# Performance work log

Measured on AMD Instinct MI355X. Metric: run time of the kernel, lower is better.

## Reference

```python
import jax, jax.numpy as jnp
import numpy as np

# ---- config (from init_kwargs) ----
PRE_NMS_THRESH = 0.05
K = 200                    # pre_nms_top_n (fixed-size top-k for jit)
NUM_CLASSES = 80
FPN_STRIDE = 8
MASK_SCALE_FACTOR = 2
MASK_STRIDE = FPN_STRIDE / MASK_SCALE_FACTOR  # 4.0
IMG_H, IMG_W = 768, 768


def setup_inputs() -> dict:
    key = jax.random.key(0)
    ks = jax.random.split(key, 6)
    N, C, H, W, DIM = 2, NUM_CLASSES, 96, 96, 32
    # FCOS-style locations for the stride-8 level: center of each cell
    ys, xs = jnp.meshgrid(jnp.arange(H, dtype=jnp.float32),
                          jnp.arange(W, dtype=jnp.float32), indexing='ij')
    locations = jnp.stack([xs.reshape(-1), ys.reshape(-1)], axis=1) * FPN_STRIDE + FPN_STRIDE // 2
    return {
        'locations': locations,                                                 # [HW, 2]
        'box_cls': jax.random.normal(ks[0], (N, C, H, W), jnp.float32) - 2.0,   # mostly below thresh
        'box_regression': jax.random.uniform(ks[1], (N, 4, H, W), jnp.float32) * 100.0,
        'centerness': jax.random.normal(ks[2], (N, 1, H, W), jnp.float32),
        'proposal_embed': jax.random.normal(ks[3], (N, DIM, H, W), jnp.float32),
        'proposal_margin': jax.random.uniform(ks[4], (N, 1, H, W), jnp.float32, minval=0.1, maxval=2.0),
        'pixel_embed': jax.random.normal(ks[5], (N, DIM, 192, 192), jnp.float32),
    }


def reference(locations, box_cls, box_regression, centerness,
              proposal_embed, proposal_margin, pixel_embed):
    N, C, H, W = box_cls.shape
    DIM = proposal_embed.shape[1]
    o_h = pixel_embed.shape[2] * MASK_SCALE_FACTOR
    o_w = pixel_embed.shape[3] * MASK_SCALE_FACTOR

    # interpolate(pixel_embed, size=(o_h, o_w), mode='bilinear', align_corners=False)
    pix_up = jax.image.resize(pixel_embed, (N, DIM, o_h, o_w), method='bilinear')

    # NCHW -> [N, HW, C] flattening (matches permute(0,2,3,1).reshape)
    scores = jax.nn.sigmoid(jnp.transpose(box_cls.reshape(N, C, H * W), (0, 2, 1)))   # [N, HW, C]
    ctr = jax.nn.sigmoid(centerness.reshape(N, H * W))                                # [N, HW]
    reg = jnp.transpose(box_regression.reshape(N, 4, H * W), (0, 2, 1))               # [N, HW, 4]
    emb = jnp.transpose(proposal_embed.reshape(N, DIM, H * W), (0, 2, 1))             # [N, HW, DIM]
    mar = proposal_margin.reshape(N, H * W)                                           # [N, HW]

    xs = jnp.arange(o_w, dtype=jnp.float32)
    ys = jnp.arange(o_h, dtype=jnp.float32)

    def per_image(s, c, r, e, m, pix):
        # threshold + centerness-weighted score; invalid candidates rank last
        cand = s > PRE_NMS_THRESH                       # [HW, C]
        sc = s * c[:, None]                             # [HW, C]
        flat = jnp.where(cand, sc, -1.0).reshape(-1)    # [HW*C]
        topv, topi = jax.lax.top_k(flat, K)             # fixed-size top-k
        loc_idx = topi // C                             # [K]
        labels = topi % C + 1                           # [K]
        valid = topv > 0.0                              # padded slots when < K candidates

        # box decode: [x - l, y - t, x + r, y + b], clipped to image
        loc = locations[loc_idx]                        # [K, 2]
        rr = r[loc_idx]                                 # [K, 4]
        x1 = jnp.clip(loc[:, 0] - rr[:, 0], 0.0, IMG_W - 1)
        y1 = jnp.clip(loc[:, 1] - rr[:, 1], 0.0, IMG_H - 1)
        x2 = jnp.clip(loc[:, 0] + rr[:, 2], 0.0, IMG_W - 1)
        y2 = jnp.clip(loc[:, 1] + rr[:, 3], 0.0, IMG_H - 1)
        boxes = jnp.stack([x1, y1, x2, y2], axis=1)     # [K, 4]

        # boxes_to_masks at mask stride: binary inside-box masks [K, o_h, o_w]
        mb = boxes / MASK_STRIDE
        in_x = (xs[None, :] >= mb[:, 0:1]) & (xs[None, :] <= mb[:, 2:3])  # [K, o_w]
        in_y = (ys[None, :] >= mb[:, 1:2]) & (ys[None, :] <= mb[:, 3:4])  # [K, o_h]
        box_mask = in_y[:, :, None] & in_x[:, None, :]

        # pixel-embed distance mask: exp(-||pix - e_k||^2 * margin_k)
        ek = e[loc_idx]                                 # [K, DIM]
        mk = m[loc_idx]                                 # [K]
        p = pix.reshape(DIM, o_h * o_w)                 # [DIM, P]
        d2 = (jnp.sum(ek * ek, axis=1)[:, None]
              + jnp.sum(p * p, axis=0)[None, :]
              - 2.0 * ek @ p)                           # [K, P] via GEMM
        prob = jnp.exp(-d2 * mk[:, None]).reshape(K, o_h, o_w)
        masks = prob * box_mask.astype(prob.dtype) * valid[:, None, None].astype(prob.dtype)
        return masks

    masks = jax.vmap(per_image)(scores, ctr, reg, emb, mar, pix_up)  # [N, K, o_h, o_w]
    return masks
```

## Files before the change

### kernel.cpp

```cpp
#include <hip/hip_runtime.h>
#include <cmath>


namespace {
constexpr int NIMG = 2;
constexpr int NC   = 80;
constexpr int NHW  = 96 * 96;
constexpr int NCHW = NC * NHW;
constexpr int NDIM = 32;
constexpr int PH = 192, PW = 192;
constexpr int OH = 384, OW = 384;
constexpr int KTOP = 200;
constexpr int CAP = 4096;
constexpr int MCAP = 1024;
constexpr int LCAP = 512;
constexpr float PRE_THRESH = 0.05f;
constexpr unsigned KEY_ZERO = 0x80000000u;
constexpr float IMG_MAX = 767.0f;

constexpr int NBOX = NIMG * KTOP;
constexpr int ZTILES = 3;
constexpr int NZB = NBOX * ZTILES;
constexpr int TILE_ROWS = 128;

constexpr int NF4 = NCHW / 4;
constexpr int SEL_BLOCKS = 128;
constexpr int SEL_STRIDE = SEL_BLOCKS * 256;
constexpr int SEL_ITERS = (NF4 + SEL_STRIDE - 1) / SEL_STRIDE;

constexpr int WS_HIST1 = 0;
constexpr int WS_CNT   = 4096;
constexpr int WS_BAR   = 4128;
constexpr int WS_TICK  = 4160;
constexpr int WS_ZERO_WORDS = 4224;
constexpr int WS_PAIRS = 4224;
constexpr int WS_PARAMS = WS_PAIRS + NIMG * CAP * 2;
constexpr int PARAM_WORDS = 40;

typedef float f4 __attribute__((ext_vector_type(4)));
}

__device__ __forceinline__ unsigned key_of(float f) {
  unsigned u = __float_as_uint(f);
  return (u & 0x80000000u) ? ~u : (u | 0x80000000u);
}
__device__ __forceinline__ unsigned aget(const unsigned* p) {
  return __hip_atomic_load(p, __ATOMIC_RELAXED, __HIP_MEMORY_SCOPE_AGENT);
}
__device__ __forceinline__ void aput(unsigned* p, unsigned v) {
  __hip_atomic_store(p, v, __ATOMIC_RELAXED, __HIP_MEMORY_SCOPE_AGENT);
}

__global__ __launch_bounds__(256) void k_zero_ws(unsigned* __restrict__ ws) {
  for (int j = threadIdx.x; j < WS_ZERO_WORDS; j += 256) aput(ws + j, 0u);
}

__global__ __launch_bounds__(256) void k_select(
    const float* __restrict__ box_cls, const float* __restrict__ ctrness,
    const float* __restrict__ locations, const float* __restrict__ box_reg,
    const float* __restrict__ pemb, const float* __restrict__ pmar,
    unsigned* __restrict__ ws) {
  __shared__ unsigned hist[2048];
  __shared__ unsigned sh_sum[256];
  __shared__ int sh_bk[2];
  __shared__ unsigned loc[LCAP][2];
  __shared__ int lcnt;
  __shared__ unsigned gbase;
  __shared__ int sh_last;
  const int t = threadIdx.x;
  const int n = blockIdx.x >= SEL_BLOCKS;
  const int bi = blockIdx.x - n * SEL_BLOCKS;

  for (int i = t; i < 2048; i += 256) hist[i] = 0;
  __syncthreads();
  const float* cls = box_cls + n * NCHW;
  const float* ctr = ctrness + n * NHW;
  unsigned kk[SEL_ITERS][4];
  #pragma unroll
  for (int s = 0; s < SEL_ITERS; ++s) {
    const int j4 = s * SEL_STRIDE + bi * 256 + t;
    if (j4 < NF4) {
      const int j = j4 * 4;
      const int c = j / NHW;
      const int hw = j - c * NHW;
      const f4 xv = *reinterpret_cast<const f4*>(cls + j);
      const f4 cv = *reinterpret_cast<const f4*>(ctr + hw);
      #pragma unroll
      for (int q = 0; q < 4; ++q) {
        const float sg = 1.0f / (1.0f + expf(-xv[q]));
        float v = -1.0f;
        if (sg > PRE_THRESH) v = sg * (1.0f / (1.0f + expf(-cv[q])));
        const unsigned k = key_of(v);
        kk[s][q] = k;
        if (k > KEY_ZERO) atomicAdd(&hist[k >> 21], 1u);
      }
    } else {
      #pragma unroll
      for (int q = 0; q < 4; ++q) kk[s][q] = 0u;
    }
  }
  __syncthreads();
  {
    unsigned* gh = ws + WS_HIST1 + n * 2048;
    for (int i = t; i < 2048; i += 256) { unsigned v = hist[i]; if (v) atomicAdd(&gh[i], v); }
  }

  __syncthreads();
  if (t == 0) {
    atomicAdd(ws + WS_BAR, 1u);
    while (aget(ws + WS_BAR) < (unsigned)(2 * SEL_BLOCKS)) __builtin_amdgcn_s_sleep(2);
  }
  __syncthreads();

  if (t == 0) { sh_bk[0] = -1; sh_bk[1] = KTOP; }
  {
    const unsigned* gh = ws + WS_HIST1 + n * 2048;
    unsigned local = 0;
    for (int j = 0; j < 8; ++j) { unsigned v = aget(gh + t * 8 + j); hist[t * 8 + j] = v; local += v; }
    sh_sum[t] = local;
  }
  __syncthreads();
  {
    unsigned S = 0;
    for (int j = t + 1; j < 256; ++j) S += sh_sum[j];
    int cand_b = -1;
    unsigned cand_above = 0;
    unsigned run = S;
    for (int j = 7; j >= 0; --j) {
      const unsigned cv = hist[t * 8 + j];
      if (cand_b < 0 && run + cv >= (unsigned)KTOP) { cand_b = t * 8 + j; cand_above = run; }
      run += cv;
    }
    if (cand_b >= 0) atomicMax(&sh_bk[0], cand_b);
    __syncthreads();
    if (cand_b >= 0 && cand_b == sh_bk[0]) sh_bk[1] = KTOP - (int)cand_above;
    __syncthreads();
  }
  const unsigned b1 = (unsigned)(sh_bk[0] < 0 ? 0 : sh_bk[0]);
  int krem = sh_bk[1];

  if (t == 0) lcnt = 0;
  __syncthreads();
  #pragma unroll
  for (int s = 0; s < SEL_ITERS; ++s) {
    #pragma unroll
    for (int q = 0; q < 4; ++q) {
      const unsigned k = kk[s][q];
      if ((k >> 21) < b1) continue;
      const int j = (s * SEL_STRIDE + bi * 256 + t) * 4 + q;
      const int c = j / NHW;
      const int hw = j - c * NHW;
      const int p = atomicAdd(&lcnt, 1);
      if (p < LCAP) { loc[p][0] = k; loc[p][1] = (unsigned)(hw * NC + c); }
    }
  }
  __syncthreads();
  const int lc = min(lcnt, LCAP);
  if (t == 0) gbase = atomicAdd(ws + WS_CNT + n, (unsigned)lc);
  __syncthreads();
  for (int i = t; i < lc; i += 256) {
    const unsigned pos = gbase + (unsigned)i;
    if (pos < (unsigned)CAP) {
      aput(&ws[WS_PAIRS + (n * CAP + (int)pos) * 2], loc[i][0]);
      aput(&ws[WS_PAIRS + (n * CAP + (int)pos) * 2 + 1], loc[i][1]);
    }
  }

  __syncthreads();
  if (t == 0) {
    const unsigned old = atomicAdd(ws + WS_TICK + n, 1u);
    sh_last = (old == (unsigned)(SEL_BLOCKS - 1)) ? 1 : 0;
  }
  __syncthreads();
  if (!sh_last) return;

  __shared__ uint2 P[CAP];
  __shared__ unsigned h256[256];
  __shared__ unsigned mKey[MCAP], mRef[MCAP];
  __shared__ int sh_b, sh_t;
  for (int s = t; s < KTOP; s += 256) aput(&ws[WS_PARAMS + (n * KTOP + s) * PARAM_WORDS], 0u);
  const int cnt = min((int)aget(ws + WS_CNT + n), CAP);
  for (int i = t; i < cnt; i += 256) {
    P[i].x = aget(&ws[WS_PAIRS + (n * CAP + i) * 2]);
    P[i].y = aget(&ws[WS_PAIRS + (n * CAP + i) * 2 + 1]);
  }
  __syncthreads();

  unsigned prefix = b1;
  int shift = 21;
  #pragma unroll
  for (int level = 0; level < 2; ++level) {
    const int newshift = shift - 8;
    h256[t] = 0;
    if (t == 0) sh_b = 0;
    __syncthreads();
    for (int i = t; i < cnt; i += 256) {
      const unsigned k = P[i].x;
      if ((k >> shift) == prefix) atomicAdd(&h256[(k >> newshift) & 255u], 1u);
    }
    __syncthreads();
    const unsigned hv = h256[t];
    unsigned S = 0;
    for (int j = t + 1; j < 256; ++j) S += h256[j];
    if (S + hv >= (unsigned)krem) atomicMax(&sh_b, t);
    __syncthreads();
    const int b = sh_b;
    if (t == b) sh_t = krem - (int)S;
    __syncthreads();
    krem = sh_t;
    prefix = (prefix << 8) | (unsigned)b;
    shift = newshift;
    __syncthreads();
  }

  if (t == 0) sh_t = 0;
  __syncthreads();
  for (int i = t; i < cnt; i += 256) {
    const unsigned k = P[i].x;
    if ((k >> 5) >= prefix) {
      const int pos = atomicAdd(&sh_t, 1);
      if (pos < MCAP) { mKey[pos] = k; mRef[pos] = P[i].y; }
    }
  }
  __syncthreads();
  const int m = min(sh_t, MCAP);

  for (int i = t; i < m; i += 256) {
    const unsigned ki = mKey[i], ri = mRef[i];
    int rank = 0;
    for (int j = 0; j < m; ++j) {
      const unsigned kj = mKey[j], rj = mRef[j];
      rank += (kj > ki || (kj == ki && rj < ri)) ? 1 : 0;
    }
    if (rank >= KTOP) continue;
    unsigned* pp = ws + WS_PARAMS + (n * KTOP + rank) * PARAM_WORDS;
    int valid = 0;
    if (ki > KEY_ZERO) {
      const int hw = (int)ri / NC;
      const float lx = locations[2 * hw], ly = locations[2 * hw + 1];
      const float rl = box_reg[(n * 4 + 0) * NHW + hw];
      const float rt = box_reg[(n * 4 + 1) * NHW + hw];
      const float rr = box_reg[(n * 4 + 2) * NHW + hw];
      const float rb = box_reg[(n * 4 + 3) * NHW + hw];
      const float x1 = fminf(fmaxf(lx - rl, 0.f), IMG_MAX);
      const float y1 = fminf(fmaxf(ly - rt, 0.f), IMG_MAX);
      const float x2 = fminf(fmaxf(lx + rr, 0.f), IMG_MAX);
      const float y2 = fminf(fmaxf(ly + rb, 0.f), IMG_MAX);
      const int ix0 = max(0, (int)ceilf(x1 * 0.25f));
      const int ix1 = min(OW - 1, (int)floorf(x2 * 0.25f));
      const int iy0 = max(0, (int)ceilf(y1 * 0.25f));
      const int iy1 = min(OH - 1, (int)floorf(y2 * 0.25f));
      if (ix0 <= ix1 && iy0 <= iy1) {
        valid = 1;
        aput(pp + 1, (unsigned)ix0); aput(pp + 2, (unsigned)ix1);
        aput(pp + 3, (unsigned)iy0); aput(pp + 4, (unsigned)iy1);
        aput(pp + 5, __float_as_uint(pmar[n * NHW + hw]));
        #pragma unroll
        for (int d = 0; d < NDIM; ++d)
          aput(pp + 8 + d, __float_as_uint(pemb[(n * NDIM + d) * NHW + hw]));
      }
    }
    aput(pp + 0, (unsigned)valid);
  }
}

__global__ __launch_bounds__(256) void k_out(const float* __restrict__ pix,
                                             const unsigned* __restrict__ ws,
                                             float* __restrict__ out) {
  const int bid = blockIdx.x;
  const int t = threadIdx.x;
  if (bid >= NBOX) {
    const int zb = bid - NBOX;
    const int nk = zb / ZTILES;
    const int rt = zb - nk * ZTILES;
    const int y0 = rt * TILE_ROWS;
    const unsigned* meta = ws + WS_PARAMS + nk * PARAM_WORDS;
    f4* ob4 = reinterpret_cast<f4*>(out + (size_t)nk * (OH * OW)) + y0 * (OW / 4);
    const f4 z = {0.f, 0.f, 0.f, 0.f};
    int qa = 0, qb = -1, iy0 = 0, iy1 = -1;
    bool overlap = false;
    if (meta[0]) {
      iy0 = (int)meta[3]; iy1 = (int)meta[4];
      if (iy1 >= y0 && iy0 < y0 + TILE_ROWS) {
        overlap = true;
        qa = (int)meta[1] >> 2;
        qb = (int)meta[2] >> 2;
      }
    }
    constexpr int F4 = TILE_ROWS * OW / 4;
    if (!overlap) {
      #pragma unroll
      for (int i = 0; i < F4 / 256; ++i)
        __builtin_nontemporal_store(z, ob4 + i * 256 + t);
    } else {
      for (int i = 0; i < F4 / 256; ++i) {
        const int idx = i * 256 + t;
        const int y = y0 + idx / 96;
        const int q = idx - (idx / 96) * 96;
        if (y >= iy0 && y <= iy1 && q >= qa && q <= qb) continue;
        __builtin_nontemporal_store(z, ob4 + idx);
      }
    }
    return;
  }

  const int nk = bid;
  const unsigned* meta = ws + WS_PARAMS + nk * PARAM_WORDS;
  if (meta[0] == 0u) return;
  const int ix0 = (int)meta[1], ix1 = (int)meta[2];
  const int iy0 = (int)meta[3], iy1 = (int)meta[4];
  const int xp0 = (ix0 >> 2) << 2;
  const int xp1 = (ix1 >> 2) * 4 + 3;
  const float margin = __uint_as_float(meta[5]);
  float e[NDIM];
  {
    const float4* e4 = reinterpret_cast<const float4*>(meta + 8);
    #pragma unroll
    for (int q = 0; q < NDIM / 4; ++q) {
      const float4 v = e4[q];
      e[4 * q + 0] = v.x; e[4 * q + 1] = v.y; e[4 * q + 2] = v.z; e[4 * q + 3] = v.w;
    }
  }
  const int n = nk / KTOP;
  const float* peb = pix + (size_t)n * NDIM * PH * PW;
  float* ob = out + (size_t)nk * (OH * OW);

  const int tx = t & 63;
  const int ts = t >> 6;
  const int h = iy1 - iy0 + 1;
  const int shh = (h + 3) >> 2;
  const int ybeg = iy0 + ts * shh;
  const int yend = min(iy0 + (ts + 1) * shh, iy1 + 1);

  for (int c = xp0 + tx; c <= xp1; c += 64) {
    const bool inx = (c >= ix0) && (c <= ix1);
    const float sx = 0.5f * (float)c - 0.25f;
    const float xf = floorf(sx);
    const float fx = sx - xf;
    const int xs0 = max((int)xf, 0);
    const int xs1 = min((int)xf + 1, PW - 1);
    float qa_[NDIM], qb_[NDIM];
    int ra = -9, rb = -9;
    for (int y = ybeg; y < yend; ++y) {
      float val = 0.f;
      if (inx) {
        const float sy = 0.5f * (float)y - 0.25f;
        const float yf = floorf(sy);
        const float fy = sy - yf;
        const int ys0 = max((int)yf, 0);
        const int ys1 = min((int)yf + 1, PH - 1);
        if (ys0 != ra) {
          if (ys0 == rb) {
            #pragma unroll
            for (int d = 0; d < NDIM; ++d) qa_[d] = qb_[d];
          } else {
            const float* p = peb + (size_t)ys0 * PW;
            #pragma unroll
            for (int d = 0; d < NDIM; ++d)
              qa_[d] = (1.f - fx) * p[d * PH * PW + xs0] + fx * p[d * PH * PW + xs1];
          }
          ra = ys0;
        }
        if (ys1 != rb) {
          if (ys1 == ra) {
            #pragma unroll
            for (int d = 0; d < NDIM; ++d) qb_[d] = qa_[d];
          } else {
            const float* p = peb + (size_t)ys1 * PW;
            #pragma unroll
            for (int d = 0; d < NDIM; ++d)
              qb_[d] = (1.f - fx) * p[d * PH * PW + xs0] + fx * p[d * PH * PW + xs1];
          }
          rb = ys1;
        }
        float d2 = 0.f;
        #pragma unroll
        for (int d = 0; d < NDIM; ++d) {
          const float pv = qa_[d] + fy * (qb_[d] - qa_[d]);
          const float df = e[d] - pv;
          d2 = fmaf(df, df, d2);
        }
        val = expf(-d2 * margin);
      }
      ob[(size_t)y * OW + c] = val;
    }
  }
}

extern "C" void kernel_launch(void* const* d_in, const int* in_sizes, int n_in,
                              void* d_out, int out_size, void* d_ws, size_t ws_size,
                              hipStream_t stream) {
  const float* locations = (const float*)d_in[0];
  const float* box_cls   = (const float*)d_in[1];
  const float* box_reg   = (const float*)d_in[2];
  const float* ctrness   = (const float*)d_in[3];
  const float* pemb      = (const float*)d_in[4];
  const float* pmar      = (const float*)d_in[5];
  const float* pix       = (const float*)d_in[6];
  float* out = (float*)d_out;
  unsigned* ws = (unsigned*)d_ws;

  k_zero_ws<<<dim3(1), dim3(256), 0, stream>>>(ws);
  k_select <<<dim3(2 * SEL_BLOCKS), dim3(256), 0, stream>>>(
      box_cls, ctrness, locations, box_reg, pemb, pmar, ws);
  k_out    <<<dim3(NBOX + NZB), dim3(256), 0, stream>>>(pix, ws, out);
}
```

Baseline: 123.7 us.

## Split output into full zero-fill pass followed by box-only mask kernel

Replaces the combined kernel, which wrote zeros only outside each box region (with per-element overlap checks) alongside the box compute blocks, with a separate grid-stride kernel that zeroes the whole output and a second kernel that writes only the in-box pixels. This removes the branchy overlap logic and the padded column handling in the box kernel. The cost is that box regions are written twice, plain stores replace nontemporal ones, and the fill can no longer overlap with box compute because it now runs in a separate launch.

```diff
diff --git a/kernel.cpp b/kernel.cpp
--- a/kernel.cpp
+++ b/kernel.cpp
@@ -19,9 +19,6 @@
 constexpr float IMG_MAX = 767.0f;
 
 constexpr int NBOX = NIMG * KTOP;
-constexpr int ZTILES = 3;
-constexpr int NZB = NBOX * ZTILES;
-constexpr int TILE_ROWS = 128;
 
 constexpr int NF4 = NCHW / 4;
 constexpr int SEL_BLOCKS = 128;
@@ -264,53 +261,22 @@
   }
 }
 
-__global__ __launch_bounds__(256) void k_out(const float* __restrict__ pix,
+__global__ __launch_bounds__(256) void k_fill(f4* __restrict__ out, int n4) {
+  const f4 z = {0.f, 0.f, 0.f, 0.f};
+  const int stride = gridDim.x * 256;
+  for (int i = blockIdx.x * 256 + threadIdx.x; i < n4; i += stride)
+    out[i] = z;
+}
+
+__global__ __launch_bounds__(256) void k_box(const float* __restrict__ pix,
                                              const unsigned* __restrict__ ws,
                                              float* __restrict__ out) {
-  const int bid = blockIdx.x;
+  const int nk = blockIdx.x;
   const int t = threadIdx.x;
-  if (bid >= NBOX) {
-    const int zb = bid - NBOX;
-    const int nk = zb / ZTILES;
-    const int rt = zb - nk * ZTILES;
-    const int y0 = rt * TILE_ROWS;
-    const unsigned* meta = ws + WS_PARAMS + nk * PARAM_WORDS;
-    f4* ob4 = reinterpret_cast<f4*>(out + (size_t)nk * (OH * OW)) + y0 * (OW / 4);
-    const f4 z = {0.f, 0.f, 0.f, 0.f};
-    int qa = 0, qb = -1, iy0 = 0, iy1 = -1;
-    bool overlap = false;
-    if (meta[0]) {
-      iy0 = (int)meta[3]; iy1 = (int)meta[4];
-      if (iy1 >= y0 && iy0 < y0 + TILE_ROWS) {
-        overlap = true;
-        qa = (int)meta[1] >> 2;
-        qb = (int)meta[2] >> 2;
-      }
-    }
-    constexpr int F4 = TILE_ROWS * OW / 4;
-    if (!overlap) {
-      #pragma unroll
-      for (int i = 0; i < F4 / 256; ++i)
-        __builtin_nontemporal_store(z, ob4 + i * 256 + t);
-    } else {
-      for (int i = 0; i < F4 / 256; ++i) {
-        const int idx = i * 256 + t;
-        const int y = y0 + idx / 96;
-        const int q = idx - (idx / 96) * 96;
-        if (y >= iy0 && y <= iy1 && q >= qa && q <= qb) continue;
-        __builtin_nontemporal_store(z, ob4 + idx);
-      }
-    }
-    return;
-  }
-
-  const int nk = bid;
   const unsigned* meta = ws + WS_PARAMS + nk * PARAM_WORDS;
   if (meta[0] == 0u) return;
   const int ix0 = (int)meta[1], ix1 = (int)meta[2];
   const int iy0 = (int)meta[3], iy1 = (int)meta[4];
-  const int xp0 = (ix0 >> 2) << 2;
-  const int xp1 = (ix1 >> 2) * 4 + 3;
   const float margin = __uint_as_float(meta[5]);
   float e[NDIM];
   {
@@ -332,8 +298,7 @@
   const int ybeg = iy0 + ts * shh;
   const int yend = min(iy0 + (ts + 1) * shh, iy1 + 1);
 
-  for (int c = xp0 + tx; c <= xp1; c += 64) {
-    const bool inx = (c >= ix0) && (c <= ix1);
+  for (int c = ix0 + tx; c <= ix1; c += 64) {
     const float sx = 0.5f * (float)c - 0.25f;
     const float xf = floorf(sx);
     const float fx = sx - xf;
@@ -342,47 +307,43 @@
     float qa_[NDIM], qb_[NDIM];
     int ra = -9, rb = -9;
     for (int y = ybeg; y < yend; ++y) {
-      float val = 0.f;
-      if (inx) {
-        const float sy = 0.5f * (float)y - 0.25f;
-        const float yf = floorf(sy);
-        const float fy = sy - yf;
-        const int ys0 = max((int)yf, 0);
-        const int ys1 = min((int)yf + 1, PH - 1);
-        if (ys0 != ra) {
-          if (ys0 == rb) {
-            #pragma unroll
-            for (int d = 0; d < NDIM; ++d) qa_[d] = qb_[d];
-          } else {
-            const float* p = peb + (size_t)ys0 * PW;
-            #pragma unroll
-            for (int d = 0; d < NDIM; ++d)
-              qa_[d] = (1.f - fx) * p[d * PH * PW + xs0] + fx * p[d * PH * PW + xs1];
-          }
-          ra = ys0;
+      const float sy = 0.5f * (float)y - 0.25f;
+      const float yf = floorf(sy);
+      const float fy = sy - yf;
+      const int ys0 = max((int)yf, 0);
+      const int ys1 = min((int)yf + 1, PH - 1);
+      if (ys0 != ra) {
+        if (ys0 == rb) {
+          #pragma unroll
+          for (int d = 0; d < NDIM; ++d) qa_[d] = qb_[d];
+        } else {
+          const float* p = peb + (size_t)ys0 * PW;
+          #pragma unroll
+          for (int d = 0; d < NDIM; ++d)
+            qa_[d] = (1.f - fx) * p[d * PH * PW + xs0] + fx * p[d * PH * PW + xs1];
         }
-        if (ys1 != rb) {
-          if (ys1 == ra) {
-            #pragma unroll
-            for (int d = 0; d < NDIM; ++d) qb_[d] = qa_[d];
-          } else {
-            const float* p = peb + (size_t)ys1 * PW;
-            #pragma unroll
-            for (int d = 0; d < NDIM; ++d)
-              qb_[d] = (1.f - fx) * p[d * PH * PW + xs0] + fx * p[d * PH * PW + xs1];
-          }
-          rb = ys1;
+        ra = ys0;
+      }
+      if (ys1 != rb) {
+        if (ys1 == ra) {
+          #pragma unroll
+          for (int d = 0; d < NDIM; ++d) qb_[d] = qa_[d];
+        } else {
+          const float* p = peb + (size_t)ys1 * PW;
+          #pragma unroll
+          for (int d = 0; d < NDIM; ++d)
+            qb_[d] = (1.f - fx) * p[d * PH * PW + xs0] + fx * p[d * PH * PW + xs1];
         }
-        float d2 = 0.f;
-        #pragma unroll
-        for (int d = 0; d < NDIM; ++d) {
-          const float pv = qa_[d] + fy * (qb_[d] - qa_[d]);
-          const float df = e[d] - pv;
-          d2 = fmaf(df, df, d2);
-        }
-        val = expf(-d2 * margin);
-      }
-      ob[(size_t)y * OW + c] = val;
+        rb = ys1;
+      }
+      float d2 = 0.f;
+      #pragma unroll
+      for (int d = 0; d < NDIM; ++d) {
+        const float pv = qa_[d] + fy * (qb_[d] - qa_[d]);
+        const float df = e[d] - pv;
+        d2 = fmaf(df, df, d2);
+      }
+      ob[(size_t)y * OW + c] = expf(-d2 * margin);
     }
   }
 }
@@ -403,5 +364,7 @@
   k_zero_ws<<<dim3(1), dim3(256), 0, stream>>>(ws);
   k_select <<<dim3(2 * SEL_BLOCKS), dim3(256), 0, stream>>>(
       box_cls, ctrness, locations, box_reg, pemb, pmar, ws);
-  k_out    <<<dim3(NBOX + NZB), dim3(256), 0, stream>>>(pix, ws, out);
-}
+  const int n4 = out_size / 4;
+  k_fill   <<<dim3(2048), dim3(256), 0, stream>>>((f4*)out, n4);
+  k_box    <<<dim3(NBOX), dim3(256), 0, stream>>>(pix, ws, out);
+}
```

Result: slower. 129.3 us (+4.6%).
